# Kernel optimization log

Measured on AMD Instinct MI355X. Metric: run time of the kernel, lower is better.

Reference implementation:

```python
import jax, jax.numpy as jnp
import numpy as np

N_S, N_H, N_ACT, N_LINKS = 512, 256, 7, 9
AXIS_LIST = jnp.array([2, 0, 2, 2, 2, 0, 2])
LINK_LIST = jnp.arange(N_ACT)
ROT_SIGN = jnp.array([1., 1., 1., 1., -1., 1., 1.], dtype=jnp.float32)  # rot[..., 4] *= -1
MASS = jnp.array([105.98, 105.98, 314.98, 279.2, 105.98, 105.98, 243.66], dtype=jnp.float32)
TOTAL_MASS = jnp.sum(MASS) + 100000.0 + 243.66
DIAGS = jnp.array([[12.19, 12.19, 3.061], [12.19, 12.19, 3.061], [15.41, 2094.71, 2103.19],
                   [9.522, 1966.28, 1966.28], [8.305, 3.061, 8.0386], [12.13, 12.13, 3.061],
                   [9.336, 44.41, 44.41]], dtype=jnp.float32)
INERTIAL = DIAGS[:, :, None] * jnp.eye(3, dtype=jnp.float32)          # (7,3,3) diagonal inertias
SUM_MASS = jnp.cumsum(MASS[::-1])[::-1].reshape(1, 1, 1, N_ACT)       # suffix sums
SUM_INERTIAL = jnp.cumsum(INERTIAL[::-1], axis=0)[::-1]               # (7,3,3)
TRIL = jnp.tril(jnp.ones((N_ACT, N_ACT), dtype=jnp.float32)).reshape(1, 1, N_ACT, 1, N_ACT)
MASS_MASK = MASS.reshape(1, 1, N_ACT, 1, 1) * TRIL                    # mass_H_wphi_mask
TF0 = jnp.array([[1, 0, 0, 0], [0, -1, 0, 0], [0, 0, 1.3, 6], [0, 0, 0, 1]], dtype=jnp.float32)
COM0 = jnp.array([[1, 0, 0, 0], [0, 1, 0, 0], [0, 0, 1, 0.5], [0, 0, 0, 1]], dtype=jnp.float32)
BASE_COM = (TF0 @ COM0)[:3, 3] * 243.66 / (100000.0 + 243.66)


def _skew(p):
    x, y, z = p[..., 0], p[..., 1], p[..., 2]
    z0 = jnp.zeros_like(x)
    return jnp.stack([jnp.stack([z0, -z, y], -1),
                      jnp.stack([z, z0, -x], -1),
                      jnp.stack([-y, x, z0], -1)], -2)


def _skew_mul(p):
    x, y, z = p[..., 0], p[..., 1], p[..., 2]
    r2 = x * x + y * y + z * z
    row0 = jnp.stack([r2 - x * x, -x * y, -x * z], -1)
    row1 = jnp.stack([-x * y, r2 - y * y, -y * z], -1)
    row2 = jnp.stack([-x * z, -y * z, r2 - z * z], -1)
    return jnp.stack([row0, row1, row2], -2)


def _inv3(H):
    a, b, c = H[..., 0, 0], H[..., 0, 1], H[..., 0, 2]
    d, e, f = H[..., 1, 0], H[..., 1, 1], H[..., 1, 2]
    g, h, i = H[..., 2, 0], H[..., 2, 1], H[..., 2, 2]
    det = a * (e * i - f * h) - b * (d * i - f * g) + c * (d * h - e * g)
    C11 = e * i - f * h; C12 = -(b * i - c * h); C13 = b * f - c * e
    C21 = -(d * i - f * g); C22 = a * i - c * g; C23 = -(a * f - c * d)
    C31 = d * h - e * g; C32 = -(a * h - b * g); C33 = a * e - b * d
    adj = jnp.stack([jnp.stack([C11, C21, C31], -1),
                     jnp.stack([C12, C22, C32], -1),
                     jnp.stack([C13, C23, C33], -1)], -2)
    return adj / det[..., None, None]


def _forward(com_list, link_pose_list, bm):
    rot = link_pose_list[:, :, :3, AXIS_LIST, LINK_LIST] * ROT_SIGN  # (n,h,3,7)
    if bm:
        del_p = com_list[:, :, :, :N_ACT] - link_pose_list[:, :, :3, 3, :N_ACT]  # (n,h,3,7)
        del_p_a = jnp.swapaxes(del_p, -1, -2)                                     # (n,h,7,3)
        del_p_skew = _skew(del_p_a)                                               # (n,h,7,3,3)
        jacob_t = jnp.cross(rot, del_p, axis=2)                                   # (n,h,3,7)
        jacob_tw = jacob_t * SUM_MASS
        H_w = jnp.sum(INERTIAL.reshape(1, 1, N_ACT, 3, 3)
                      + MASS.reshape(1, 1, N_ACT, 1, 1) * _skew_mul(del_p_a), axis=2)  # (n,h,3,3)
        term1 = jnp.einsum('aij,shja->shia', SUM_INERTIAL, rot)                   # (n,h,3,7)
        jac_w = jacob_t[:, :, None] * MASS_MASK                                   # (n,h,7,3,7)
        term2 = jnp.einsum('shaij,shajk->shik', del_p_skew, jac_w)                # (n,h,3,7)
        H_wphi = term1 + term2
        system_com = jnp.einsum('ntci,i->ntc', com_list, MASS) / TOTAL_MASS       # (n,h,3)
        r_og = _skew(system_com - BASE_COM)                                       # (n,h,3,3)
        H_s = TOTAL_MASS * (r_og @ r_og) + H_w
        H_theta = H_wphi - r_og @ jacob_tw
        H_inv = _inv3(H_s)
        top = -(jacob_tw / TOTAL_MASS + r_og @ (H_inv @ H_theta))
        bot = -(H_inv @ H_theta)
        return jnp.concatenate([top, bot], axis=2)                                # (n,h,6,7)
    else:
        del_p = link_pose_list[:, :, :3, 3, -2][..., None] - link_pose_list[:, :, :3, 3, :N_ACT]
        jt = jnp.cross(rot, del_p, axis=2)
        return jnp.concatenate([jt, rot], axis=2)


def setup_inputs() -> dict:
    key = jax.random.key(0)
    k1, k2 = jax.random.split(key)
    com_list = jax.random.normal(k1, (N_S, N_H, 3, N_ACT), dtype=jnp.float32)
    link_pose_list = jax.random.normal(k2, (N_S, N_H, 4, 4, N_LINKS), dtype=jnp.float32)
    return {"com_list": com_list, "link_pose_list": link_pose_list, "bm": 1}


def reference(com_list, link_pose_list, bm):
    return _forward(com_list, link_pose_list, bm)
```

## Files before the change

kernel.cpp:

```cpp
#include <hip/hip_runtime.h>


#define BLK 128
#define IT_F4 23

__global__ __launch_bounds__(BLK) void canadarm_jacob_kernel(
    const float* __restrict__ com,
    const float* __restrict__ pose,
    const int* __restrict__ bm_ptr,
    float* __restrict__ out,
    int n_items)
{
    __shared__ float4 lds4[BLK * IT_F4];

    const int tid = threadIdx.x;
    const int item0 = blockIdx.x * BLK;

    const float MASS[7] = {105.98f, 105.98f, 314.98f, 279.2f, 105.98f, 105.98f, 243.66f};
    const float SUMM[7] = {1261.76f, 1155.78f, 1049.80f, 734.82f, 455.62f, 349.64f, 243.66f};
    const float SIX[7] = {79.083f, 66.893f, 54.703f, 39.293f, 29.771f, 21.466f, 9.336f};
    const float SIY[7] = {4144.971f, 4132.781f, 4120.591f, 2025.881f, 59.601f, 56.540f, 44.410f};
    const float SIZ[7] = {4131.1016f, 4128.0406f, 4124.9796f, 2021.7896f, 55.5096f, 47.471f, 44.410f};
    const float TM     = 101505.42f;
    const float INV_TM = 1.0f / 101505.42f;
    const float BCZ    = 6.65f * 243.66f / 100243.66f;

    {
        const float4* Pb = reinterpret_cast<const float4*>(pose) + (size_t)item0 * 36;
#pragma unroll
        for (int it = 0; it < 28; ++it) {
            const int c = it * BLK + tid;
            const int item = c / 28;
            const int off = c - item * 28;
            const float4 v = Pb[item * 36 + off];
            const int r = off / 9;
            const int oo = off - r * 9;
            const bool live = (r < 3) && (oo < 2 || oo >= 4);
            const int slot = 7 * r + (oo < 2 ? oo : oo - 2);
            if (live) lds4[item * IT_F4 + slot] = v;
        }
    }
    __syncthreads();

    const float4* L = &lds4[tid * IT_F4];
    float rot[3][7];
    float tr[3][8];
#pragma unroll
    for (int r = 0; r < 3; ++r) {
        const float4 q0 = L[7 * r + 0];
        const float4 q1 = L[7 * r + 1];
        const float4 q4 = L[7 * r + 2];
        const float4 q5 = L[7 * r + 3];
        const float4 q6 = L[7 * r + 4];
        const float4 q7 = L[7 * r + 5];
        const float4 q8 = L[7 * r + 6];
        rot[r][0] = q4.z;
        rot[r][1] = q0.y;
        rot[r][2] = q5.x;
        rot[r][3] = q5.y;
        rot[r][4] = -q5.z;
        rot[r][5] = q1.y;
        rot[r][6] = q6.x;
        tr[r][0] = q6.w;
        tr[r][1] = q7.x; tr[r][2] = q7.y; tr[r][3] = q7.z; tr[r][4] = q7.w;
        tr[r][5] = q8.x; tr[r][6] = q8.y; tr[r][7] = q8.z;
    }

    const int bm = bm_ptr[0];
    float o[42];

    if (bm) {
        const float* C = com + (size_t)(item0 + tid) * 21;
        float cm[3][7];
#pragma unroll
        for (int r = 0; r < 3; ++r)
#pragma unroll
            for (int i = 0; i < 7; ++i) cm[r][i] = C[r * 7 + i];

        float scx = 0.f, scy = 0.f, scz = 0.f;
#pragma unroll
        for (int i = 0; i < 7; ++i) {
            scx += cm[0][i] * MASS[i];
            scy += cm[1][i] * MASS[i];
            scz += cm[2][i] * MASS[i];
        }
        const float vx = scx * INV_TM;
        const float vy = scy * INV_TM;
        const float vz = scz * INV_TM - BCZ;

        float dp[3][7], jt[3][7];
        float hxx = SIX[0], hyy = SIY[0], hzz = SIZ[0];
        float hxy = 0.f, hxz = 0.f, hyz = 0.f;
#pragma unroll
        for (int i = 0; i < 7; ++i) {
            const float x = cm[0][i] - tr[0][i];
            const float y = cm[1][i] - tr[1][i];
            const float z = cm[2][i] - tr[2][i];
            dp[0][i] = x; dp[1][i] = y; dp[2][i] = z;
            jt[0][i] = rot[1][i] * z - rot[2][i] * y;
            jt[1][i] = rot[2][i] * x - rot[0][i] * z;
            jt[2][i] = rot[0][i] * y - rot[1][i] * x;
            const float m = MASS[i];
            hxx += m * (y * y + z * z);
            hyy += m * (x * x + z * z);
            hzz += m * (x * x + y * y);
            hxy -= m * x * y;
            hxz -= m * x * z;
            hyz -= m * y * z;
        }

        float wx[7], wy[7], wz[7];
        wx[6] = MASS[6] * dp[0][6];
        wy[6] = MASS[6] * dp[1][6];
        wz[6] = MASS[6] * dp[2][6];
#pragma unroll
        for (int k = 5; k >= 0; --k) {
            wx[k] = wx[k + 1] + MASS[k] * dp[0][k];
            wy[k] = wy[k + 1] + MASS[k] * dp[1][k];
            wz[k] = wz[k + 1] + MASS[k] * dp[2][k];
        }

        const float vv = vx * vx + vy * vy + vz * vz;
        const float a  = hxx + TM * (vx * vx - vv);
        const float b  = hxy + TM * (vx * vy);
        const float c  = hxz + TM * (vx * vz);
        const float e  = hyy + TM * (vy * vy - vv);
        const float f  = hyz + TM * (vy * vz);
        const float i9 = hzz + TM * (vz * vz - vv);

        const float c11 = e * i9 - f * f;
        const float c12 = c * f - b * i9;
        const float c13 = b * f - e * c;
        const float det = a * c11 + b * c12 + c * c13;
        const float rdet = 1.0f / det;
        const float i00 = c11 * rdet;
        const float i01 = c12 * rdet;
        const float i02 = c13 * rdet;
        const float i11 = (a * i9 - c * c) * rdet;
        const float i12 = (c * b - a * f) * rdet;
        const float i22 = (a * e - b * b) * rdet;

#pragma unroll
        for (int k = 0; k < 7; ++k) {
            const float ux = wx[k] - SUMM[k] * vx;
            const float uy = wy[k] - SUMM[k] * vy;
            const float uz = wz[k] - SUMM[k] * vz;
            const float jx = jt[0][k], jy = jt[1][k], jz = jt[2][k];
            const float htx = SIX[k] * rot[0][k] + uy * jz - uz * jy;
            const float hty = SIY[k] * rot[1][k] + uz * jx - ux * jz;
            const float htz = SIZ[k] * rot[2][k] + ux * jy - uy * jx;
            const float bx = i00 * htx + i01 * hty + i02 * htz;
            const float by = i01 * htx + i11 * hty + i12 * htz;
            const float bz = i02 * htx + i12 * hty + i22 * htz;
            const float s = SUMM[k] * INV_TM;
            o[0 * 7 + k] = -(s * jx + vy * bz - vz * by);
            o[1 * 7 + k] = -(s * jy + vz * bx - vx * bz);
            o[2 * 7 + k] = -(s * jz + vx * by - vy * bx);
            o[3 * 7 + k] = -bx;
            o[4 * 7 + k] = -by;
            o[5 * 7 + k] = -bz;
        }
    } else {
#pragma unroll
        for (int k = 0; k < 7; ++k) {
            const float dx = tr[0][7] - tr[0][k];
            const float dy = tr[1][7] - tr[1][k];
            const float dz = tr[2][7] - tr[2][k];
            o[0 * 7 + k] = rot[1][k] * dz - rot[2][k] * dy;
            o[1 * 7 + k] = rot[2][k] * dx - rot[0][k] * dz;
            o[2 * 7 + k] = rot[0][k] * dy - rot[1][k] * dx;
            o[3 * 7 + k] = rot[0][k];
            o[4 * 7 + k] = rot[1][k];
            o[5 * 7 + k] = rot[2][k];
        }
    }

    __syncthreads();
    float* ldsf = reinterpret_cast<float*>(lds4);
#pragma unroll
    for (int j = 0; j < 42; ++j) ldsf[tid * 42 + j] = o[j];
    __syncthreads();

    {
        float4* Ob4 = reinterpret_cast<float4*>(out) + (size_t)blockIdx.x * (BLK * 42 / 4);
        const float4* Lf4 = reinterpret_cast<const float4*>(ldsf);
#pragma unroll
        for (int i = 0; i < 10; ++i) Ob4[tid + i * BLK] = Lf4[tid + i * BLK];
        if (tid < BLK * 42 / 4 - 10 * BLK)
            Ob4[tid + 10 * BLK] = Lf4[tid + 10 * BLK];
    }
}

extern "C" void kernel_launch(void* const* d_in, const int* in_sizes, int n_in,
                              void* d_out, int out_size, void* d_ws, size_t ws_size,
                              hipStream_t stream) {
    const float* com  = (const float*)d_in[0];
    const float* pose = (const float*)d_in[1];
    const int*   bm   = (const int*)d_in[2];
    float* out = (float*)d_out;

    const int n_items = in_sizes[0] / 21;
    const int grid = n_items / BLK;
    canadarm_jacob_kernel<<<grid, BLK, 0, stream>>>(com, pose, bm, out, n_items);
}
```

Baseline: 149.1 us.

## Stage pose and com loads directly into LDS via global_load_lds with smaller blocks

Replaces register-staged pose gathering with direct global-to-LDS async loads (global_load_lds, 16 bytes per lane) that fetch only the needed float4s. The com array is now also staged through LDS with coalesced float4 loads instead of per-thread strided scalar reads. Block size is halved to 64 with launch_bounds min-blocks of 1. This is meant to cut register pressure and uncoalesced traffic, but it relies on the builtin's LDS addressing semantics (wave-uniform base plus lane offset), which makes the per-item layout easy to get wrong.

```diff
diff --git a/kernel.cpp b/kernel.cpp
--- a/kernel.cpp
+++ b/kernel.cpp
@@ -1,17 +1,19 @@
 #include <hip/hip_runtime.h>
 
 
-#define BLK 128
-#define IT_F4 23
-
-__global__ __launch_bounds__(BLK) void canadarm_jacob_kernel(
+#define BLK 64
+
+typedef const __attribute__((address_space(1))) void GAS;
+typedef __attribute__((address_space(3))) void LAS;
+
+__global__ __launch_bounds__(BLK, 1) void canadarm_jacob_kernel(
     const float* __restrict__ com,
     const float* __restrict__ pose,
     const int* __restrict__ bm_ptr,
-    float* __restrict__ out,
-    int n_items)
+    float* __restrict__ out)
 {
-    __shared__ float4 lds4[BLK * IT_F4];
+    __shared__ float4 pose_lds[BLK * 21];
+    __shared__ float4 com_lds[384];
 
     const int tid = threadIdx.x;
     const int item0 = blockIdx.x * BLK;
@@ -26,23 +28,35 @@
     const float BCZ    = 6.65f * 243.66f / 100243.66f;
 
     {
-        const float4* Pb = reinterpret_cast<const float4*>(pose) + (size_t)item0 * 36;
-#pragma unroll
-        for (int it = 0; it < 28; ++it) {
-            const int c = it * BLK + tid;
-            const int item = c / 28;
-            const int off = c - item * 28;
-            const float4 v = Pb[item * 36 + off];
-            const int r = off / 9;
-            const int oo = off - r * 9;
-            const bool live = (r < 3) && (oo < 2 || oo >= 4);
-            const int slot = 7 * r + (oo < 2 ? oo : oo - 2);
-            if (live) lds4[item * IT_F4 + slot] = v;
-        }
-    }
+        const float4* Pb4 = reinterpret_cast<const float4*>(pose) + (size_t)item0 * 36;
+#pragma unroll
+        for (int i = 0; i < 21; ++i) {
+            const int d    = i * BLK + tid;
+            const int item = d / 21;
+            const int li   = d - item * 21;
+            const int r    = li / 7;
+            const int q    = li - r * 7;
+            const int off  = 9 * r + (q < 2 ? q : q + 2);
+            __builtin_amdgcn_global_load_lds(
+                (GAS*)(Pb4 + item * 36 + off),
+                (LAS*)(pose_lds + i * BLK), 16, 0, 0);
+        }
+        const float4* Cb4 = reinterpret_cast<const float4*>(com) + (size_t)item0 * 21 / 4 * 4 / 4;
+        const float4* Cb4x = reinterpret_cast<const float4*>(com + (size_t)item0 * 21);
+#pragma unroll
+        for (int i = 0; i < 6; ++i) {
+            const int d  = i * BLK + tid;
+            const int dc = d < 336 ? d : 335;
+            __builtin_amdgcn_global_load_lds(
+                (GAS*)(Cb4x + dc),
+                (LAS*)(com_lds + i * BLK), 16, 0, 0);
+        }
+        (void)Cb4;
+    }
+    asm volatile("s_waitcnt vmcnt(0)" ::: "memory");
     __syncthreads();
 
-    const float4* L = &lds4[tid * IT_F4];
+    const float4* L = &pose_lds[tid * 21];
     float rot[3][7];
     float tr[3][8];
 #pragma unroll
@@ -70,12 +84,12 @@
     float o[42];
 
     if (bm) {
-        const float* C = com + (size_t)(item0 + tid) * 21;
+        const float* Cf = reinterpret_cast<const float*>(com_lds) + tid * 21;
         float cm[3][7];
 #pragma unroll
         for (int r = 0; r < 3; ++r)
 #pragma unroll
-            for (int i = 0; i < 7; ++i) cm[r][i] = C[r * 7 + i];
+            for (int i = 0; i < 7; ++i) cm[r][i] = Cf[r * 7 + i];
 
         float scx = 0.f, scy = 0.f, scz = 0.f;
 #pragma unroll
@@ -176,7 +190,7 @@
     }
 
     __syncthreads();
-    float* ldsf = reinterpret_cast<float*>(lds4);
+    float* ldsf = reinterpret_cast<float*>(pose_lds);
 #pragma unroll
     for (int j = 0; j < 42; ++j) ldsf[tid * 42 + j] = o[j];
     __syncthreads();
@@ -186,7 +200,7 @@
         const float4* Lf4 = reinterpret_cast<const float4*>(ldsf);
 #pragma unroll
         for (int i = 0; i < 10; ++i) Ob4[tid + i * BLK] = Lf4[tid + i * BLK];
-        if (tid < BLK * 42 / 4 - 10 * BLK)
+        if (tid < 672 - 10 * BLK)
             Ob4[tid + 10 * BLK] = Lf4[tid + 10 * BLK];
     }
 }
@@ -201,5 +215,5 @@
 
     const int n_items = in_sizes[0] / 21;
     const int grid = n_items / BLK;
-    canadarm_jacob_kernel<<<grid, BLK, 0, stream>>>(com, pose, bm, out, n_items);
+    canadarm_jacob_kernel<<<grid, BLK, 0, stream>>>(com, pose, bm, out);
 }
```

New measurement: 124.4 us. 16.6% less time.
